# Performance work log

Hardware: AMD Instinct MI355X
Metric: run time of the kernel (lower is better)

## Reference

```python
import jax, jax.numpy as jnp
import numpy as np

T = 2048; H = 1024; NH = 16; NKV = 4; HD = 64
E = 32; TOPK = 4; NG = 4; TG = 2; IM = 384; ISH = 384
ROT = HD // 2          # partial_rotary_factor = 0.5
EPS = 1e-5; RSF = 1.0; THETA = 10000.0


def setup_inputs() -> dict:
    ks = jax.random.split(jax.random.key(0), 12)
    g = lambda k, sh, sc=0.02: jax.random.normal(k, sh, jnp.float32) * sc
    return {
        "hidden_states": g(ks[0], (T, H), 1.0),
        "residual": g(ks[1], (T, H), 1.0),
        "in_ln_w": jnp.ones((H,), jnp.float32),
        "post_ln_w": jnp.ones((H,), jnp.float32),
        "q_norm_w": jnp.ones((HD,), jnp.float32),
        "k_norm_w": jnp.ones((HD,), jnp.float32),
        "Wqkv": g(ks[2], (H, (NH + 2 * NKV) * HD)),
        "Wo": g(ks[3], (NH * HD, H)),
        "Wg": g(ks[4], (H, E)),
        "gate_bias": g(ks[5], (E,), 0.1),
        "Wgu": g(ks[6], (E, H, 2 * IM)),
        "Wd": g(ks[7], (E, IM, H)),
        "Wgu_sh": g(ks[8], (H, 2 * ISH)),
        "Wd_sh": g(ks[9], (ISH, H)),
        "positions": jnp.arange(T, dtype=jnp.int32),
    }


def _rms(x, w):
    return x * jax.lax.rsqrt(jnp.mean(x * x, -1, keepdims=True) + EPS) * w


def _rope(x, pos):
    # neox-style rotary on the first ROT dims of each head; x: [T, nheads, HD]
    half = ROT // 2
    inv = THETA ** (-(jnp.arange(half, dtype=jnp.float32) * 2.0 / ROT))
    ang = pos.astype(jnp.float32)[:, None] * inv          # [T, half]
    c = jnp.cos(ang)[:, None, :]
    s = jnp.sin(ang)[:, None, :]
    x1, x2, rest = x[..., :half], x[..., half:ROT], x[..., ROT:]
    return jnp.concatenate([x1 * c - x2 * s, x1 * s + x2 * c, rest], -1)


def _layer(pos, hidden, residual, in_ln_w, post_ln_w, q_norm_w, k_norm_w,
           Wqkv, Wo, Wg, gate_bias, Wgu, Wd, Wgu_sh, Wd_sh):
    # fused add-RMSNorm (vllm RMSNorm(x, residual))
    residual = hidden + residual
    hidden = _rms(residual, in_ln_w)

    # self-attention (GQA, per-head qk-norm, partial rotary, causal)
    qkv = hidden @ Wqkv
    q = qkv[:, :NH * HD].reshape(T, NH, HD)
    k = qkv[:, NH * HD:(NH + NKV) * HD].reshape(T, NKV, HD)
    v = qkv[:, (NH + NKV) * HD:].reshape(T, NKV, HD)
    q = _rms(q, q_norm_w)
    k = _rms(k, k_norm_w)
    q = _rope(q, pos)
    k = _rope(k, pos)
    rep = NH // NKV
    k = jnp.repeat(k, rep, axis=1)
    v = jnp.repeat(v, rep, axis=1)
    scores = jnp.einsum('thd,shd->hts', q, k) * (HD ** -0.5)
    causal = pos[:, None] >= pos[None, :]
    scores = jnp.where(causal[None], scores, -jnp.inf)
    attn = jax.nn.softmax(scores, axis=-1)
    o = jnp.einsum('hts,shd->thd', attn, v).reshape(T, NH * HD)
    hidden = o @ Wo

    # post-attention fused add-RMSNorm
    residual = hidden + residual
    hidden = _rms(residual, post_ln_w)

    # --- Glm4MoE: grouped sigmoid top-k router with e_score_correction_bias ---
    logits = hidden.astype(jnp.float32) @ Wg            # gate runs in fp32
    scr = jax.nn.sigmoid(logits)                        # [T, E]
    sfc = scr + gate_bias                               # scores_for_choice
    # group score = sum of top-2 biased scores within each group
    gs = jnp.sum(jax.lax.top_k(sfc.reshape(T, NG, E // NG), 2)[0], -1)  # [T, NG]
    _, gidx = jax.lax.top_k(gs, TG)
    gmask = jnp.zeros((T, NG), jnp.float32).at[jnp.arange(T)[:, None], gidx].set(1.0)
    emask = jnp.repeat(gmask, E // NG, axis=1)          # [T, E]
    _, ids = jax.lax.top_k(jnp.where(emask > 0, sfc, -jnp.inf), TOPK)
    w = jnp.take_along_axis(scr, ids, axis=1)           # weights from unbiased scores
    w = w / jnp.sum(w, -1, keepdims=True)               # renormalize (norm_topk_prob)
    wdense = jnp.zeros((T, E), jnp.float32).at[jnp.arange(T)[:, None], ids].set(w)

    # routed experts: dense-over-experts reference for the grouped GEMM dispatch
    gu = jnp.einsum('th,ehi->tei', hidden, Wgu)         # [T, E, 2*IM]
    act = jax.nn.silu(gu[..., :IM]) * gu[..., IM:]      # SiluAndMul
    routed = jnp.einsum('te,tei,eih->th', wdense, act, Wd)

    # shared expert MLP
    gus = hidden @ Wgu_sh
    shared = (jax.nn.silu(gus[:, :ISH]) * gus[:, ISH:]) @ Wd_sh

    hidden = routed * RSF + shared
    return hidden, residual


def reference(hidden_states, residual, in_ln_w, post_ln_w, q_norm_w, k_norm_w,
              Wqkv, Wo, Wg, gate_bias, Wgu, Wd, Wgu_sh, Wd_sh, positions):
    return _layer(positions, hidden_states, residual, in_ln_w, post_ln_w,
                  q_norm_w, k_norm_w, Wqkv, Wo, Wg, gate_bias, Wgu, Wd,
                  Wgu_sh, Wd_sh)
```

## Files before the change

kernel.cpp:

```cpp
#include <hip/hip_runtime.h>
#include <math.h>

#define TT 2048
#define HH 1024
#define NHEADS 16
#define NKVH 4
#define HDIM 64
#define NEXP 32
#define TOPK_ 4
#define NGRP 4
#define IMID 384
#define ISHARED 384
#define QKV_W (24*64)
#define EPS_ 1e-5f
#define MAXSB 288
#define NSPLITS 80

typedef __attribute__((ext_vector_type(8))) short short8;
typedef __attribute__((ext_vector_type(4))) float f32x4;

__device__ __forceinline__ ushort f2bf(float x) {
  union { float f; unsigned u; } v; v.f = x;
  unsigned r = v.u + 0x7fffu + ((v.u >> 16) & 1u);
  return (ushort)(r >> 16);
}
__device__ __forceinline__ float bf2f(ushort u) {
  union { unsigned i; float f; } v; v.i = (unsigned)u << 16; return v.f;
}

__device__ __forceinline__ void gload16(const void* g, void* l) {
  __builtin_amdgcn_global_load_lds(
      (const __attribute__((address_space(1))) unsigned int*)g,
      (__attribute__((address_space(3))) unsigned int*)l, 16, 0, 0);
}

__device__ __forceinline__ short8 read_a_frag32(const ushort* As, int lg, int row) {
  return *(const short8*)(As + ((lg * 32 + (row ^ lg)) * 8));
}
__device__ __forceinline__ short8 read_a_frag64(const ushort* As, int lg, int row) {
  return *(const short8*)(As + ((lg * 64 + (row ^ lg)) * 8));
}
__device__ __forceinline__ short8 read_b_frag(const ushort* Bs, int lg, int col) {
  int boff = (col * 16) ^ (((col >> 3) & 7) << 4);
  return *(const short8*)((const char*)Bs + lg * 1024 + boff);
}

__device__ __forceinline__ void stage_B_tile(const float* __restrict__ B, int ldb,
                                             int k0, int col0, ushort* Bs, int tid) {
  int a = tid >> 4;
  int cG = tid & 15;
  int k = 2 * a;
  const float* p0 = B + (size_t)(k0 + k) * ldb + col0 + cG * 4;
  const float* p1 = p0 + ldb;
  float4 r0 = *(const float4*)p0;
  float4 r1 = *(const float4*)p1;
  int gg = (k & 15) >> 2;
  int slot = (k & 3) + ((k >> 4) << 2);
  float v0[4] = {r0.x, r0.y, r0.z, r0.w};
  float v1[4] = {r1.x, r1.y, r1.z, r1.w};
  char* plane = (char*)Bs + gg * 1024;
  #pragma unroll
  for (int j = 0; j < 4; ++j) {
    int c = cG * 4 + j;
    unsigned pk = (unsigned)f2bf(v0[j]) | ((unsigned)f2bf(v1[j]) << 16);
    int boff = ((c * 16) ^ (((c >> 3) & 7) << 4)) + slot * 2;
    *(unsigned*)(plane + boff) = pk;
  }
}

__global__ __launch_bounds__(256) void pack_B_kernel(
    const float* __restrict__ src, ushort* __restrict__ dst, int N) {
  __shared__ ushort tileB[2048];
  int tid = threadIdx.x;
  stage_B_tile(src, N, blockIdx.y * 32, blockIdx.x * 64, tileB, tid);
  __syncthreads();
  size_t toff = ((size_t)blockIdx.y * gridDim.x + blockIdx.x) * 2048;
  *(short8*)(dst + toff + tid * 8) = *(const short8*)(tileB + tid * 8);
}

__global__ __launch_bounds__(256) void gemm64_bb(
    const ushort* __restrict__ Ab, const ushort* __restrict__ Bpk,
    float* __restrict__ C, int M, int N, int K) {
  __shared__ ushort As[4][2048];
  __shared__ ushort Bs[4][2048];
  int tid = threadIdx.x;
  int row0 = blockIdx.y * 64, col0 = blockIdx.x * 64;
  int ntn = N >> 6;
  int wid = tid >> 6, lane = tid & 63;
  int lg = lane >> 4, lr = lane & 15;
  int wrow = (wid >> 1) * 32, wcol = (wid & 1) * 32;
  const ushort* asrc = Ab + (size_t)(row0 + (lane ^ wid)) * K + wid * 8;
  const ushort* bsrc = Bpk + (size_t)blockIdx.x * 2048 + wid * 512 + lane * 8;
  const int NT = K >> 5;
  f32x4 acc[2][2] = {};

  auto issue = [&](int tt) {
    int b = tt & 3;
    gload16(asrc + tt * 32, &As[b][wid * 512]);
    gload16(bsrc + (size_t)tt * ntn * 2048, &Bs[b][wid * 512]);
  };
  issue(0); issue(1); issue(2);
  for (int t = 0; t < NT; ++t) {
    int ahead = NT - 1 - t;
    if (ahead >= 2)      asm volatile("s_waitcnt vmcnt(4)" ::: "memory");
    else if (ahead == 1) asm volatile("s_waitcnt vmcnt(2)" ::: "memory");
    else                 asm volatile("s_waitcnt vmcnt(0)" ::: "memory");
    __builtin_amdgcn_s_barrier();
    if (t + 3 < NT) issue(t + 3);
    int cb = t & 3;
    short8 af0 = read_a_frag64(&As[cb][0], lg, wrow + lr);
    short8 af1 = read_a_frag64(&As[cb][0], lg, wrow + 16 + lr);
    #pragma unroll
    for (int nn = 0; nn < 2; ++nn) {
      short8 bf_ = read_b_frag(&Bs[cb][0], lg, wcol + nn * 16 + lr);
      acc[0][nn] = __builtin_amdgcn_mfma_f32_16x16x32_bf16(af0, bf_, acc[0][nn], 0, 0, 0);
      acc[1][nn] = __builtin_amdgcn_mfma_f32_16x16x32_bf16(af1, bf_, acc[1][nn], 0, 0, 0);
    }
  }
  #pragma unroll
  for (int mm = 0; mm < 2; ++mm)
    #pragma unroll
    for (int nn = 0; nn < 2; ++nn) {
      int row = row0 + wrow + mm * 16 + lg * 4;
      int col = col0 + wcol + nn * 16 + lr;
      #pragma unroll
      for (int i = 0; i < 4; ++i)
        C[(size_t)(row + i) * N + col] = acc[mm][nn][i];
    }
}

__global__ __launch_bounds__(256) void moe_up_pk(
    const ushort* __restrict__ hln2b, const ushort* __restrict__ Wpk,
    const int* __restrict__ perm, const int* __restrict__ offs,
    const int* __restrict__ counts, const int* __restrict__ sb_e,
    const int* __restrict__ sb_base, const int* __restrict__ nsb,
    ushort* __restrict__ actb) {
  int b = blockIdx.x;
  int sb = ((b & 7) * 36) + (b >> 3);
  if (sb >= *nsb) return;
  int e = sb_e[sb];
  int base = sb_base[sb];
  int start = offs[e];
  int nt = min(32, counts[e] - base);
  __shared__ int tokmap[32];
  int tid = threadIdx.x;
  if (tid < 32) tokmap[tid] = perm[start + base + ((tid < nt) ? tid : 0)] >> 2;
  __shared__ ushort As[3][1024];
  __shared__ ushort Bg[3][2048];
  __shared__ ushort Bu[3][2048];
  __syncthreads();
  int bz = blockIdx.y, col0 = bz * 64;
  int wid = tid >> 6, lane = tid & 63;
  int lg = lane >> 4, lr = lane & 15;
  int wrow = (wid >> 1) * 16, wcol = (wid & 1) * 32;
  const ushort* bgt = Wpk + ((size_t)(e * 32) * 12 + bz) * 2048 + wid * 512 + lane * 8;
  const ushort* but = bgt + (size_t)6 * 2048;
  int ga = wid * 2 + (lane >> 5);
  const ushort* asrcA = hln2b + (size_t)tokmap[(lane & 31) ^ ga] * HH + ga * 8;
  const int NT = HH >> 5;
  f32x4 accg[2] = {}, accu[2] = {};

  auto issue = [&](int tt) {
    int bb = tt % 3;
    if (wid < 2) gload16(asrcA + tt * 32, &As[bb][wid * 1024 / 2]);
    gload16(bgt + (size_t)tt * 12 * 2048, &Bg[bb][wid * 512]);
    gload16(but + (size_t)tt * 12 * 2048, &Bu[bb][wid * 512]);
  };
  issue(0); issue(1);
  for (int t = 0; t < NT; ++t) {
    if (t < NT - 1) {
      if (wid < 2) asm volatile("s_waitcnt vmcnt(3)" ::: "memory");
      else         asm volatile("s_waitcnt vmcnt(2)" ::: "memory");
    } else {
      asm volatile("s_waitcnt vmcnt(0)" ::: "memory");
    }
    __builtin_amdgcn_s_barrier();
    if (t + 2 < NT) issue(t + 2);
    int cb = t % 3;
    short8 af = read_a_frag32(&As[cb][0], lg, wrow + lr);
    #pragma unroll
    for (int nn = 0; nn < 2; ++nn) {
      short8 bgf = read_b_frag(&Bg[cb][0], lg, wcol + nn * 16 + lr);
      short8 buf_ = read_b_frag(&Bu[cb][0], lg, wcol + nn * 16 + lr);
      accg[nn] = __builtin_amdgcn_mfma_f32_16x16x32_bf16(af, bgf, accg[nn], 0, 0, 0);
      accu[nn] = __builtin_amdgcn_mfma_f32_16x16x32_bf16(af, buf_, accu[nn], 0, 0, 0);
    }
  }
  #pragma unroll
  for (int nn = 0; nn < 2; ++nn) {
    int pcol = col0 + ((wid & 1) << 5) + ((lr >> 2) << 3) + (nn << 2) + (lr & 3);
    #pragma unroll
    for (int i = 0; i < 4; ++i) {
      int rr = wrow + lg * 4 + i;
      if (rr < nt) {
        float gv = accg[nn][i], uv = accu[nn][i];
        float av = gv / (1.f + expf(-gv)) * uv;
        actb[(size_t)(start + base + rr) * IMID + pcol] = f2bf(av);
      }
    }
  }
}

__global__ __launch_bounds__(256) void moe_down_pk(
    const ushort* __restrict__ actb, const ushort* __restrict__ Wpk,
    const int* __restrict__ offs, const int* __restrict__ counts,
    const int* __restrict__ sb_e, const int* __restrict__ sb_base,
    const int* __restrict__ nsb, ushort* __restrict__ partialb) {
  int b = blockIdx.x;
  int sb = ((b & 7) * 36) + (b >> 3);
  if (sb >= *nsb) return;
  int e = sb_e[sb];
  int base = sb_base[sb];
  int start = offs[e];
  int nt = min(32, counts[e] - base);
  __shared__ ushort As[3][1024];
  __shared__ ushort Bs[3][2048];
  int tid = threadIdx.x;
  int bz = blockIdx.y, col0 = bz * 64;
  int wid = tid >> 6, lane = tid & 63;
  int lg = lane >> 4, lr = lane & 15;
  int wrow = (wid >> 1) * 16, wcol = (wid & 1) * 32;
  const ushort* bt0 = Wpk + ((size_t)(e * 12) * 16 + bz) * 2048 + wid * 512 + lane * 8;
  int ga = wid * 2 + (lane >> 5);
  const ushort* asrcA = actb + (size_t)(start + base + ((lane & 31) ^ ga)) * IMID + ga * 8;
  const int NT = IMID >> 5;
  f32x4 acc[2] = {};

  auto issue = [&](int tt) {
    int bb = tt % 3;
    if (wid < 2) gload16(asrcA + tt * 32, &As[bb][wid * 512]);
    gload16(bt0 + (size_t)tt * 16 * 2048, &Bs[bb][wid * 512]);
  };
  issue(0); issue(1);
  for (int t = 0; t < NT; ++t) {
    if (t < NT - 1) {
      if (wid < 2) asm volatile("s_waitcnt vmcnt(2)" ::: "memory");
      else         asm volatile("s_waitcnt vmcnt(1)" ::: "memory");
    } else {
      asm volatile("s_waitcnt vmcnt(0)" ::: "memory");
    }
    __builtin_amdgcn_s_barrier();
    if (t + 2 < NT) issue(t + 2);
    int cb = t % 3;
    short8 af = read_a_frag32(&As[cb][0], lg, wrow + lr);
    #pragma unroll
    for (int nn = 0; nn < 2; ++nn) {
      short8 bf_ = read_b_frag(&Bs[cb][0], lg, wcol + nn * 16 + lr);
      acc[nn] = __builtin_amdgcn_mfma_f32_16x16x32_bf16(af, bf_, acc[nn], 0, 0, 0);
    }
  }
  #pragma unroll
  for (int nn = 0; nn < 2; ++nn)
    #pragma unroll
    for (int i = 0; i < 4; ++i) {
      int rr = wrow + lg * 4 + i;
      if (rr < nt)
        partialb[(size_t)(start + base + rr) * HH + col0 + wcol + nn * 16 + lr] = f2bf(acc[nn][i]);
    }
}

__global__ __launch_bounds__(256) void add_rms_kernel(
    const float* __restrict__ a, const float* __restrict__ b,
    const float* __restrict__ w, float* __restrict__ sum_out,
    float* __restrict__ ln_out, ushort* __restrict__ lnb) {
  int t = blockIdx.x, tid = threadIdx.x;
  float4 x = reinterpret_cast<const float4*>(a + (size_t)t*HH)[tid];
  float4 y = reinterpret_cast<const float4*>(b + (size_t)t*HH)[tid];
  x.x += y.x; x.y += y.y; x.z += y.z; x.w += y.w;
  float ss = x.x*x.x + x.y*x.y + x.z*x.z + x.w*x.w;
  #pragma unroll
  for (int off = 1; off < 64; off <<= 1) ss += __shfl_xor(ss, off);
  __shared__ float wsum[4];
  int wid = tid >> 6, lane = tid & 63;
  if (lane == 0) wsum[wid] = ss;
  __syncthreads();
  float tot = wsum[0] + wsum[1] + wsum[2] + wsum[3];
  float r = rsqrtf(tot * (1.0f/HH) + EPS_);
  reinterpret_cast<float4*>(sum_out + (size_t)t*HH)[tid] = x;
  float4 wl = reinterpret_cast<const float4*>(w)[tid];
  float4 o = make_float4(x.x*r*wl.x, x.y*r*wl.y, x.z*r*wl.z, x.w*r*wl.w);
  reinterpret_cast<float4*>(ln_out + (size_t)t*HH)[tid] = o;
  ushort4 ub;
  ub.x = f2bf(o.x); ub.y = f2bf(o.y); ub.z = f2bf(o.z); ub.w = f2bf(o.w);
  int dst = ((tid >> 3) << 5) + ((tid & 3) << 3) + (((tid >> 2) & 1) << 2);
  *(ushort4*)(lnb + (size_t)t * HH + dst) = ub;
}

__global__ __launch_bounds__(256) void qk_norm_rope_kernel(
    float* __restrict__ qkv, const float* __restrict__ qw,
    const float* __restrict__ kw, const int* __restrict__ pos) {
  int t = blockIdx.x;
  int hh = blockIdx.y * 4 + (threadIdx.x >> 6);
  int lane = threadIdx.x & 63;
  float* p = qkv + (size_t)t * QKV_W + hh * HDIM;
  float x = p[lane];
  float ss = x * x;
  #pragma unroll
  for (int off = 1; off < 64; off <<= 1) ss += __shfl_xor(ss, off);
  float r = rsqrtf(ss * (1.0f/HDIM) + EPS_);
  float wv = (hh < NHEADS ? qw : kw)[lane];
  float xn = x * r * wv;
  float partner = __shfl_xor(xn, 16);
  float out = xn;
  if (lane < 32) {
    int i = lane & 15;
    float inv = powf(10000.0f, -(float)i / 16.0f);
    float ang = (float)pos[t] * inv;
    float cv = cosf(ang), sv = sinf(ang);
    out = (lane < 16) ? (xn * cv - partner * sv) : (partner * sv + xn * cv);
  }
  p[lane] = out;
}

__global__ __launch_bounds__(256) void pack_KV_kernel(
    const float* __restrict__ qkv, ushort* __restrict__ Kpk,
    ushort* __restrict__ Vpk) {
  __shared__ ushort kimg[2048];
  __shared__ ushort vimg[2048];
  int tid = threadIdx.x;
  int kt = blockIdx.x, kvh = blockIdx.y;
  {
    int c = tid >> 7, t2 = tid & 127;
    int g = t2 & 3, r = t2 >> 2;
    const float* kp = qkv + (size_t)(kt*32 + r) * QKV_W + NHEADS*HDIM + kvh*HDIM + 32*c + 4*g;
    float4 h0 = *(const float4*)kp;
    float4 h1 = *(const float4*)(kp + 16);
    short8 v;
    v[0]=(short)f2bf(h0.x); v[1]=(short)f2bf(h0.y); v[2]=(short)f2bf(h0.z); v[3]=(short)f2bf(h0.w);
    v[4]=(short)f2bf(h1.x); v[5]=(short)f2bf(h1.y); v[6]=(short)f2bf(h1.z); v[7]=(short)f2bf(h1.w);
    *(short8*)(kimg + c*1024 + (g*32 + (r^g))*8) = v;
  }
  stage_B_tile(qkv + (size_t)(NHEADS+NKVH)*HDIM + (size_t)kvh*HDIM, QKV_W, kt*32, 0, vimg, tid);
  __syncthreads();
  size_t toff = ((size_t)(kvh * (TT/32) + kt)) * 2048;
  *(short8*)(Kpk + toff + tid * 8) = *(const short8*)(kimg + tid * 8);
  *(short8*)(Vpk + toff + tid * 8) = *(const short8*)(vimg + tid * 8);
}

__global__ __launch_bounds__(256) void attn_v3_kernel(
    const float* __restrict__ qkv, const ushort* __restrict__ Kpk,
    const ushort* __restrict__ Vpk, ushort* __restrict__ ob,
    float* __restrict__ po, float* __restrict__ pl) {
  __shared__ ushort Ks[3][2048];
  __shared__ ushort Vs[3][2048];
  int tid = threadIdx.x;
  int wid = tid >> 6, lane = tid & 63;
  int lg = lane >> 4, lr = lane & 15;
  int h = blockIdx.y;
  int f = blockIdx.x;
  int g = 0;
  while (f >= 4 * (g + 1) * (g + 2)) ++g;
  int r_ = f - 4 * g * (g + 1);
  int ns = g + 1;
  int qb = 8 * g + r_ / ns;
  int s = r_ % ns;
  int tiles_total = 2 * qb + 2;
  int per = (tiles_total + ns - 1) / ns;
  int lo = s * per;
  int nloc = min(per, tiles_total - lo);
  int kvh = h >> 2;
  int q0 = qb * 64 + wid * 16;
  int qg = q0 + lr;
  const float SCL = 0.125f * 1.44269504f;
  const float FM = 16.0f;

  const float* qrow = qkv + (size_t)qg * QKV_W + h * HDIM;
  short8 qfr[2];
  #pragma unroll
  for (int c = 0; c < 2; ++c) {
    float4 a = *(const float4*)(qrow + 32*c + 4*lg);
    float4 b = *(const float4*)(qrow + 32*c + 4*lg + 16);
    short8 v;
    v[0]=(short)f2bf(a.x*SCL); v[1]=(short)f2bf(a.y*SCL); v[2]=(short)f2bf(a.z*SCL); v[3]=(short)f2bf(a.w*SCL);
    v[4]=(short)f2bf(b.x*SCL); v[5]=(short)f2bf(b.y*SCL); v[6]=(short)f2bf(b.z*SCL); v[7]=(short)f2bf(b.w*SCL);
    qfr[c] = v;
  }

  const ushort* ksrc = Kpk + (size_t)(kvh * (TT/32) + lo) * 2048 + wid * 512 + lane * 8;
  const ushort* vsrc = Vpk + (size_t)(kvh * (TT/32) + lo) * 2048 + wid * 512 + lane * 8;

  f32x4 o_acc[4] = {};
  float l_st = 0.f;

  auto issue = [&](int tt) {
    int b = tt % 3;
    gload16(ksrc + (size_t)tt * 2048, &Ks[b][wid * 512]);
    gload16(vsrc + (size_t)tt * 2048, &Vs[b][wid * 512]);
  };
  issue(0);
  if (nloc > 1) issue(1);
  for (int tt = 0; tt < nloc; ++tt) {
    if (tt < nloc - 1) asm volatile("s_waitcnt vmcnt(2)" ::: "memory");
    else               asm volatile("s_waitcnt vmcnt(0)" ::: "memory");
    __builtin_amdgcn_s_barrier();
    if (tt + 2 < nloc) issue(tt + 2);
    int t = lo + tt;
    if (t * 32 > q0 + 15) continue;
    int cb = tt % 3;
    f32x4 st[2];
    #pragma unroll
    for (int n = 0; n < 2; ++n) {
      short8 kf0 = *(const short8*)(&Ks[cb][(lg*32 + ((16*n + lr) ^ lg)) * 8]);
      short8 kf1 = *(const short8*)(&Ks[cb][1024 + (lg*32 + ((16*n + lr) ^ lg)) * 8]);
      f32x4 z = {};
      z = __builtin_amdgcn_mfma_f32_16x16x32_bf16(kf0, qfr[0], z, 0, 0, 0);
      st[n] = __builtin_amdgcn_mfma_f32_16x16x32_bf16(kf1, qfr[1], z, 0, 0, 0);
    }
    float p[2][4];
    float psum = 0.f;
    if (t * 32 + 31 <= q0) {
      #pragma unroll
      for (int n = 0; n < 2; ++n)
        #pragma unroll
        for (int i = 0; i < 4; ++i) {
          float pv = exp2f(st[n][i] - FM);
          p[n][i] = pv; psum += pv;
        }
    } else {
      #pragma unroll
      for (int n = 0; n < 2; ++n)
        #pragma unroll
        for (int i = 0; i < 4; ++i) {
          int kvg = t*32 + 16*n + 4*lg + i;
          float pv = (kvg <= qg) ? exp2f(st[n][i] - FM) : 0.f;
          p[n][i] = pv; psum += pv;
        }
    }
    psum += __shfl_xor(psum, 16);
    psum += __shfl_xor(psum, 32);
    l_st += psum;
    union { unsigned u[4]; short8 s8; } pu;
    asm volatile("v_cvt_pk_bf16_f32 %0, %1, %2" : "=v"(pu.u[0]) : "v"(p[0][0]), "v"(p[0][1]));
    asm volatile("v_cvt_pk_bf16_f32 %0, %1, %2" : "=v"(pu.u[1]) : "v"(p[0][2]), "v"(p[0][3]));
    asm volatile("v_cvt_pk_bf16_f32 %0, %1, %2" : "=v"(pu.u[2]) : "v"(p[1][0]), "v"(p[1][1]));
    asm volatile("v_cvt_pk_bf16_f32 %0, %1, %2" : "=v"(pu.u[3]) : "v"(p[1][2]), "v"(p[1][3]));
    short8 pa = pu.s8;
    #pragma unroll
    for (int nd = 0; nd < 4; ++nd) {
      short8 vf = read_b_frag(&Vs[cb][0], lg, 16*nd + lr);
      o_acc[nd] = __builtin_amdgcn_mfma_f32_16x16x32_bf16(pa, vf, o_acc[nd], 0, 0, 0);
    }
  }

  if (ns == 1) {
    #pragma unroll
    for (int i = 0; i < 4; ++i) {
      float lrow = __shfl(l_st, 4*lg + i);
      float inv = 1.0f / lrow;
      int row = q0 + 4*lg + i;
      ushort* op = ob + (size_t)row * (NHEADS*HDIM) + h * HDIM;
      #pragma unroll
      for (int nd = 0; nd < 4; ++nd) {
        int pcol = ((nd >> 1) << 5) + ((lr >> 2) << 3) + ((nd & 1) << 2) + (lr & 3);
        op[pcol] = f2bf(o_acc[nd][i] * inv);
      }
    }
  } else {
    float* pob = po + ((size_t)f * NHEADS + h) * 4096;
    #pragma unroll
    for (int nd = 0; nd < 4; ++nd)
      #pragma unroll
      for (int i = 0; i < 4; ++i)
        pob[(wid * 16 + lg * 4 + i) * 64 + 16 * nd + lr] = o_acc[nd][i];
    if (lg == 0)
      pl[((size_t)f * NHEADS + h) * 64 + wid * 16 + lr] = l_st;
  }
}

__global__ __launch_bounds__(256) void attn_combine_kernel(
    const float* __restrict__ po, const float* __restrict__ pl,
    ushort* __restrict__ ob) {
  int h = blockIdx.x;
  int qb = 8 + blockIdx.y;
  int g = qb >> 3;
  int ns = g + 1;
  int f0 = 4 * g * (g + 1) + (qb - 8 * g) * ns;
  int tid = threadIdx.x;
  int r = tid >> 2, c = tid & 3;
  float acc[16] = {};
  float lsum = 0.f;
  for (int s = 0; s < ns; ++s) {
    size_t base = ((size_t)(f0 + s) * NHEADS + h) * 4096 + r * 64 + c * 16;
    #pragma unroll
    for (int j = 0; j < 4; ++j) {
      float4 v = *(const float4*)(po + base + j * 4);
      acc[j*4+0] += v.x; acc[j*4+1] += v.y; acc[j*4+2] += v.z; acc[j*4+3] += v.w;
    }
    lsum += pl[((size_t)(f0 + s) * NHEADS + h) * 64 + r];
  }
  float inv = 1.0f / lsum;
  int row = qb * 64 + r;
  ushort* op = ob + (size_t)row * (NHEADS*HDIM) + h * HDIM + (c >> 1) * 32 + (c & 1) * 4;
  #pragma unroll
  for (int a = 0; a < 4; ++a) {
    ushort4 u;
    u.x = f2bf(acc[a*4+0] * inv); u.y = f2bf(acc[a*4+1] * inv);
    u.z = f2bf(acc[a*4+2] * inv); u.w = f2bf(acc[a*4+3] * inv);
    *(ushort4*)(op + a * 8) = u;
  }
}

__global__ __launch_bounds__(256) void router_kernel(
    const float* __restrict__ hln, const float* __restrict__ Wg,
    const float* __restrict__ bias, int* __restrict__ sel_e,
    float* __restrict__ sel_w) {
  __shared__ float hid[4][HH];
  int tid = threadIdx.x, wid = tid >> 6, lane = tid & 63;
  int t = blockIdx.x * 4 + wid;
  const float4* src = (const float4*)(hln + (size_t)t * HH);
  float4* dst = (float4*)hid[wid];
  #pragma unroll
  for (int j = 0; j < 4; ++j) dst[j * 64 + lane] = src[j * 64 + lane];
  int e = lane & 31, half = lane >> 5;
  const float* wp = Wg + (size_t)(half * 512) * NEXP + e;
  const float* hp = hid[wid] + half * 512;
  float p = 0.f;
  #pragma unroll 8
  for (int h = 0; h < 512; ++h) p += hp[h] * wp[(size_t)h * NEXP];
  p += __shfl_xor(p, 32);
  float sc = 1.0f / (1.0f + expf(-p));
  float sfc = sc + bias[e];
  float m1 = sfc, m2 = -1e30f;
  #pragma unroll
  for (int off = 1; off <= 4; off <<= 1) {
    float om1 = __shfl_xor(m1, off), om2 = __shfl_xor(m2, off);
    float hi_ = fmaxf(m1, om1);
    float lo_ = fmaxf(fminf(m1, om1), fmaxf(m2, om2));
    m1 = hi_; m2 = lo_;
  }
  float gs = m1 + m2;
  float gv[4] = {__shfl(gs, 0), __shfl(gs, 8), __shfl(gs, 16), __shfl(gs, 24)};
  int g1 = 0; float b1 = gv[0];
  #pragma unroll
  for (int g = 1; g < 4; ++g) if (gv[g] > b1) { b1 = gv[g]; g1 = g; }
  int g2 = -1; float b2 = -1e30f;
  #pragma unroll
  for (int g = 0; g < 4; ++g) if (g != g1 && gv[g] > b2) { b2 = gv[g]; g2 = g; }
  bool keep = ((e >> 3) == g1) || ((e >> 3) == g2);
  float cand = keep ? sfc : -1e30f;
  int ids[4]; float wv[4]; float wsum = 0.f;
  #pragma unroll
  for (int s = 0; s < 4; ++s) {
    float v = cand; int ix = e;
    #pragma unroll
    for (int off = 1; off < 64; off <<= 1) {
      float ov = __shfl_xor(v, off); int oix = __shfl_xor(ix, off);
      if (ov > v || (ov == v && oix < ix)) { v = ov; ix = oix; }
    }
    ids[s] = ix;
    if (e == ix) cand = -1e30f;
    float w = __shfl(sc, ix);
    wv[s] = w; wsum += w;
  }
  if (lane == 0) {
    #pragma unroll
    for (int s = 0; s < 4; ++s) {
      sel_e[t * 4 + s] = ids[s];
      sel_w[t * 4 + s] = wv[s] / wsum;
    }
  }
}

__global__ __launch_bounds__(256) void count_kernel(
    const int* __restrict__ sel_e, int* __restrict__ counts) {
  int e = blockIdx.x, tid = threadIdx.x;
  int c = 0;
  for (int i = tid; i < TT * TOPK_; i += 256) c += (sel_e[i] == e);
  #pragma unroll
  for (int off = 1; off < 64; off <<= 1) c += __shfl_xor(c, off);
  __shared__ int wsum[4];
  if ((tid & 63) == 0) wsum[tid >> 6] = c;
  __syncthreads();
  if (tid == 0) counts[e] = wsum[0] + wsum[1] + wsum[2] + wsum[3];
}

__global__ void scan_kernel(const int* __restrict__ counts,
                            int* __restrict__ offs, int* __restrict__ cursor,
                            int* __restrict__ sb_e, int* __restrict__ sb_base,
                            int* __restrict__ nsb) {
  if (threadIdx.x == 0) {
    int acc = 0, n = 0;
    for (int e = 0; e < NEXP; ++e) {
      offs[e] = acc; cursor[e] = acc;
      int c = counts[e];
      for (int b = 0; b < c; b += 32) { sb_e[n] = e; sb_base[n] = b; ++n; }
      acc += c;
    }
    *nsb = n;
  }
}

__global__ void scatter_kernel(const int* __restrict__ sel_e,
                               int* __restrict__ cursor, int* __restrict__ perm,
                               int* __restrict__ ipos) {
  int i = blockIdx.x * 256 + threadIdx.x;
  if (i < TT * TOPK_) {
    int e = sel_e[i];
    int pos = atomicAdd(&cursor[e], 1);
    perm[pos] = i;
    ipos[i] = pos;
  }
}

__global__ __launch_bounds__(256) void silu_shared_kernel(
    const float* __restrict__ gus, ushort* __restrict__ shsb) {
  int i = blockIdx.x * 256 + threadIdx.x;
  if (i < TT * (ISHARED/4)) {
    int t = i / (ISHARED/4), k = i % (ISHARED/4);
    const float* gp = gus + (size_t)t * (2*ISHARED) + k * 4;
    float4 g4 = *(const float4*)gp;
    float4 u4 = *(const float4*)(gp + ISHARED);
    ushort4 r;
    r.x = f2bf(g4.x / (1.f + expf(-g4.x)) * u4.x);
    r.y = f2bf(g4.y / (1.f + expf(-g4.y)) * u4.y);
    r.z = f2bf(g4.z / (1.f + expf(-g4.z)) * u4.z);
    r.w = f2bf(g4.w / (1.f + expf(-g4.w)) * u4.w);
    int pdst = ((k >> 3) << 5) + ((k & 3) << 3) + (((k >> 2) & 1) << 2);
    *(ushort4*)(shsb + (size_t)t * ISHARED + pdst) = r;
  }
}

__global__ __launch_bounds__(256) void final_combine_kernel(
    const ushort* __restrict__ partialb, const float* __restrict__ sel_w,
    const int* __restrict__ ipos, const float* __restrict__ shared_out,
    float* __restrict__ out_hidden) {
  int t = blockIdx.x, tid = threadIdx.x;
  float w0 = sel_w[t*4], w1 = sel_w[t*4+1], w2 = sel_w[t*4+2], w3 = sel_w[t*4+3];
  int p0 = ipos[t*4], p1 = ipos[t*4+1], p2 = ipos[t*4+2], p3 = ipos[t*4+3];
  ushort4 a0 = *(const ushort4*)(partialb + (size_t)p0*HH + tid*4);
  ushort4 a1 = *(const ushort4*)(partialb + (size_t)p1*HH + tid*4);
  ushort4 a2 = *(const ushort4*)(partialb + (size_t)p2*HH + tid*4);
  ushort4 a3 = *(const ushort4*)(partialb + (size_t)p3*HH + tid*4);
  float4 sh = reinterpret_cast<const float4*>(shared_out + (size_t)t*HH)[tid];
  float4 r;
  r.x = (w0*bf2f(a0.x) + w1*bf2f(a1.x) + w2*bf2f(a2.x) + w3*bf2f(a3.x)) + sh.x;
  r.y = (w0*bf2f(a0.y) + w1*bf2f(a1.y) + w2*bf2f(a2.y) + w3*bf2f(a3.y)) + sh.y;
  r.z = (w0*bf2f(a0.z) + w1*bf2f(a1.z) + w2*bf2f(a2.z) + w3*bf2f(a3.z)) + sh.z;
  r.w = (w0*bf2f(a0.w) + w1*bf2f(a1.w) + w2*bf2f(a2.w) + w3*bf2f(a3.w)) + sh.w;
  reinterpret_cast<float4*>(out_hidden + (size_t)t*HH)[tid] = r;
}

extern "C" void kernel_launch(void* const* d_in, const int* in_sizes, int n_in,
                              void* d_out, int out_size, void* d_ws, size_t ws_size,
                              hipStream_t stream) {
  const float* hidden   = (const float*)d_in[0];
  const float* residual = (const float*)d_in[1];
  const float* in_ln_w  = (const float*)d_in[2];
  const float* post_ln_w= (const float*)d_in[3];
  const float* q_norm_w = (const float*)d_in[4];
  const float* k_norm_w = (const float*)d_in[5];
  const float* Wqkv     = (const float*)d_in[6];
  const float* Wo       = (const float*)d_in[7];
  const float* Wg       = (const float*)d_in[8];
  const float* gate_bias= (const float*)d_in[9];
  const float* Wgu      = (const float*)d_in[10];
  const float* Wd       = (const float*)d_in[11];
  const float* Wgu_sh   = (const float*)d_in[12];
  const float* Wd_sh    = (const float*)d_in[13];
  const int*   positions= (const int*)d_in[14];
  float* out = (float*)d_out;

  float* f = (float*)d_ws;
  size_t off = 0;
  float* R_A   = f + off; off += (size_t)TT*HH;
  float* HLN   = f + off; off += (size_t)TT*HH;
  float* QKV   = f + off; off += (size_t)TT*QKV_W;
  float* OATT  = f + off; off += (size_t)TT*HH;
  float* HLN2  = f + off; off += (size_t)TT*HH;
  float* SELW  = f + off; off += (size_t)TT*TOPK_;
  float* PO    = f + off; off += (size_t)NSPLITS*NHEADS*4096;
  float* PL    = f + off; off += (size_t)NSPLITS*NHEADS*64;
  ushort* HLNB  = (ushort*)(f + off); off += (size_t)TT*HH/2;
  ushort* HLN2B = (ushort*)(f + off); off += (size_t)TT*HH/2;
  ushort* OATTB = (ushort*)(f + off); off += (size_t)TT*HH/2;
  ushort* SHSB  = (ushort*)(f + off); off += (size_t)TT*ISHARED/2;
  ushort* KPK   = (ushort*)(f + off); off += (size_t)NKVH*(TT/32)*2048/2;
  ushort* VPK   = (ushort*)(f + off); off += (size_t)NKVH*(TT/32)*2048/2;
  ushort* ACTB  = (ushort*)(f + off); off += (size_t)(TT*TOPK_ + 128)*IMID/2;
  ushort* PARTB = (ushort*)(f + off); off += (size_t)TT*TOPK_*HH/2;
  ushort* PK_QKV = (ushort*)(f + off); off += (size_t)HH*QKV_W/2;
  ushort* PK_WO  = (ushort*)(f + off); off += (size_t)HH*HH/2;
  ushort* PK_WGU = (ushort*)(f + off); off += (size_t)NEXP*HH*(2*IMID)/2;
  ushort* PK_WD  = (ushort*)(f + off); off += (size_t)NEXP*IMID*HH/2;
  ushort* PK_GUSH= (ushort*)(f + off); off += (size_t)HH*(2*ISHARED)/2;
  ushort* PK_DSH = (ushort*)(f + off); off += (size_t)ISHARED*HH/2;
  int* ibase   = (int*)(f + off);
  int* SELE    = ibase;
  int* PERM    = ibase + TT*TOPK_;
  int* IPOS    = ibase + 2*TT*TOPK_;
  int* COUNTS  = ibase + 3*TT*TOPK_;
  int* OFFS    = COUNTS + NEXP;
  int* CURSOR  = OFFS + NEXP;
  int* SB_E    = CURSOR + NEXP;
  int* SB_BASE = SB_E + MAXSB;
  int* NSB     = SB_BASE + MAXSB;

  pack_B_kernel<<<dim3(QKV_W/64, HH/32), 256, 0, stream>>>(Wqkv, PK_QKV, QKV_W);
  pack_B_kernel<<<dim3(HH/64, HH/32), 256, 0, stream>>>(Wo, PK_WO, HH);
  pack_B_kernel<<<dim3((2*IMID)/64, NEXP*HH/32), 256, 0, stream>>>(Wgu, PK_WGU, 2*IMID);
  pack_B_kernel<<<dim3(HH/64, NEXP*IMID/32), 256, 0, stream>>>(Wd, PK_WD, HH);
  pack_B_kernel<<<dim3((2*ISHARED)/64, HH/32), 256, 0, stream>>>(Wgu_sh, PK_GUSH, 2*ISHARED);
  pack_B_kernel<<<dim3(HH/64, ISHARED/32), 256, 0, stream>>>(Wd_sh, PK_DSH, HH);

  add_rms_kernel<<<TT, 256, 0, stream>>>(hidden, residual, in_ln_w, R_A, HLN, HLNB);
  gemm64_bb<<<dim3(QKV_W/64, TT/64), 256, 0, stream>>>(HLNB, PK_QKV, QKV, TT, QKV_W, HH);
  qk_norm_rope_kernel<<<dim3(TT, 5), 256, 0, stream>>>(QKV, q_norm_w, k_norm_w, positions);
  pack_KV_kernel<<<dim3(TT/32, NKVH), 256, 0, stream>>>(QKV, KPK, VPK);
  attn_v3_kernel<<<dim3(NSPLITS, NHEADS), 256, 0, stream>>>(QKV, KPK, VPK, OATTB, PO, PL);
  attn_combine_kernel<<<dim3(NHEADS, 24), 256, 0, stream>>>(PO, PL, OATTB);
  gemm64_bb<<<dim3(HH/64, TT/64), 256, 0, stream>>>(OATTB, PK_WO, HLN, TT, HH, HH);
  add_rms_kernel<<<TT, 256, 0, stream>>>(HLN, R_A, post_ln_w, out + (size_t)TT*HH, HLN2, HLN2B);
  router_kernel<<<TT/4, 256, 0, stream>>>(HLN2, Wg, gate_bias, SELE, SELW);
  count_kernel<<<NEXP, 256, 0, stream>>>(SELE, COUNTS);
  scan_kernel<<<1, 64, 0, stream>>>(COUNTS, OFFS, CURSOR, SB_E, SB_BASE, NSB);
  scatter_kernel<<<(TT*TOPK_ + 255)/256, 256, 0, stream>>>(SELE, CURSOR, PERM, IPOS);
  moe_up_pk<<<dim3(MAXSB, IMID/64), 256, 0, stream>>>(HLN2B, PK_WGU, PERM, OFFS, COUNTS, SB_E, SB_BASE, NSB, ACTB);
  moe_down_pk<<<dim3(MAXSB, HH/64), 256, 0, stream>>>(ACTB, PK_WD, OFFS, COUNTS, SB_E, SB_BASE, NSB, PARTB);
  gemm64_bb<<<dim3((2*ISHARED)/64, TT/64), 256, 0, stream>>>(HLN2B, PK_GUSH, QKV, TT, 2*ISHARED, HH);
  silu_shared_kernel<<<(TT*(ISHARED/4) + 255)/256, 256, 0, stream>>>(QKV, SHSB);
  gemm64_bb<<<dim3(HH/64, TT/64), 256, 0, stream>>>(SHSB, PK_DSH, OATT, TT, HH, ISHARED);
  final_combine_kernel<<<TT, 256, 0, stream>>>(PARTB, SELW, IPOS, OATT, out);
}
```

Baseline: 350.0 us.

## Drop LDS staging in MoE expert GEMMs; load fragments directly to registers

The MoE up and down kernels no longer stage A and B tiles through triple-buffered shared memory with barriers. Each wave now reads its MFMA fragments straight from global memory into registers, with one-step register prefetch. Each wave computes a 32x32 output tile, so the grid's y-dimension is halved. This removes LDS traffic and barrier synchronisation, but each wave fetches its own copy of the A data rather than sharing it across the block, and relies on cache hits and latency hiding from register prefetch.

```diff
diff --git a/kernel.cpp b/kernel.cpp
--- a/kernel.cpp
+++ b/kernel.cpp
@@ -34,9 +34,6 @@
       (__attribute__((address_space(3))) unsigned int*)l, 16, 0, 0);
 }
 
-__device__ __forceinline__ short8 read_a_frag32(const ushort* As, int lg, int row) {
-  return *(const short8*)(As + ((lg * 32 + (row ^ lg)) * 8));
-}
 __device__ __forceinline__ short8 read_a_frag64(const ushort* As, int lg, int row) {
   return *(const short8*)(As + ((lg * 64 + (row ^ lg)) * 8));
 }
@@ -142,63 +139,66 @@
   int base = sb_base[sb];
   int start = offs[e];
   int nt = min(32, counts[e] - base);
-  __shared__ int tokmap[32];
   int tid = threadIdx.x;
-  if (tid < 32) tokmap[tid] = perm[start + base + ((tid < nt) ? tid : 0)] >> 2;
-  __shared__ ushort As[3][1024];
-  __shared__ ushort Bg[3][2048];
-  __shared__ ushort Bu[3][2048];
-  __syncthreads();
-  int bz = blockIdx.y, col0 = bz * 64;
   int wid = tid >> 6, lane = tid & 63;
   int lg = lane >> 4, lr = lane & 15;
-  int wrow = (wid >> 1) * 16, wcol = (wid & 1) * 32;
-  const ushort* bgt = Wpk + ((size_t)(e * 32) * 12 + bz) * 2048 + wid * 512 + lane * 8;
-  const ushort* but = bgt + (size_t)6 * 2048;
-  int ga = wid * 2 + (lane >> 5);
-  const ushort* asrcA = hln2b + (size_t)tokmap[(lane & 31) ^ ga] * HH + ga * 8;
-  const int NT = HH >> 5;
-  f32x4 accg[2] = {}, accu[2] = {};
-
-  auto issue = [&](int tt) {
-    int bb = tt % 3;
-    if (wid < 2) gload16(asrcA + tt * 32, &As[bb][wid * 1024 / 2]);
-    gload16(bgt + (size_t)tt * 12 * 2048, &Bg[bb][wid * 512]);
-    gload16(but + (size_t)tt * 12 * 2048, &Bu[bb][wid * 512]);
-  };
-  issue(0); issue(1);
-  for (int t = 0; t < NT; ++t) {
-    if (t < NT - 1) {
-      if (wid < 2) asm volatile("s_waitcnt vmcnt(3)" ::: "memory");
-      else         asm volatile("s_waitcnt vmcnt(2)" ::: "memory");
-    } else {
-      asm volatile("s_waitcnt vmcnt(0)" ::: "memory");
-    }
-    __builtin_amdgcn_s_barrier();
-    if (t + 2 < NT) issue(t + 2);
-    int cb = t % 3;
-    short8 af = read_a_frag32(&As[cb][0], lg, wrow + lr);
+  int bz = blockIdx.y * 2 + (wid >> 1);
+  int wcol = (wid & 1) * 32;
+  int tok0 = perm[start + base + min(lr, nt - 1)] >> 2;
+  int tok1 = perm[start + base + min(16 + lr, nt - 1)] >> 2;
+  const ushort* a0p = hln2b + (size_t)tok0 * HH + lg * 8;
+  const ushort* a1p = hln2b + (size_t)tok1 * HH + lg * 8;
+  int c0 = wcol + lr, c1 = wcol + 16 + lr;
+  int sw0 = (c0 * 16) ^ (((c0 >> 3) & 7) << 4);
+  int sw1 = (c1 * 16) ^ (((c1 >> 3) & 7) << 4);
+  const char* gbase = (const char*)Wpk + ((size_t)(e * 32) * 12 + bz) * 4096 + lg * 1024;
+  const char* ubase = gbase + (size_t)6 * 4096;
+  const size_t bstep = (size_t)12 * 4096;
+  f32x4 accg[2][2] = {}, accu[2][2] = {};
+  short8 a0c = *(const short8*)(a0p);
+  short8 a1c = *(const short8*)(a1p);
+  short8 g0c = *(const short8*)(gbase + sw0);
+  short8 g1c = *(const short8*)(gbase + sw1);
+  short8 u0c = *(const short8*)(ubase + sw0);
+  short8 u1c = *(const short8*)(ubase + sw1);
+  #pragma unroll 4
+  for (int t = 0; t < 32; ++t) {
+    short8 a0n = a0c, a1n = a1c, g0n = g0c, g1n = g1c, u0n = u0c, u1n = u1c;
+    if (t < 31) {
+      const char* gb = gbase + (size_t)(t + 1) * bstep;
+      const char* ub = ubase + (size_t)(t + 1) * bstep;
+      a0n = *(const short8*)(a0p + (t + 1) * 32);
+      a1n = *(const short8*)(a1p + (t + 1) * 32);
+      g0n = *(const short8*)(gb + sw0);
+      g1n = *(const short8*)(gb + sw1);
+      u0n = *(const short8*)(ub + sw0);
+      u1n = *(const short8*)(ub + sw1);
+    }
+    accg[0][0] = __builtin_amdgcn_mfma_f32_16x16x32_bf16(a0c, g0c, accg[0][0], 0, 0, 0);
+    accg[0][1] = __builtin_amdgcn_mfma_f32_16x16x32_bf16(a0c, g1c, accg[0][1], 0, 0, 0);
+    accg[1][0] = __builtin_amdgcn_mfma_f32_16x16x32_bf16(a1c, g0c, accg[1][0], 0, 0, 0);
+    accg[1][1] = __builtin_amdgcn_mfma_f32_16x16x32_bf16(a1c, g1c, accg[1][1], 0, 0, 0);
+    accu[0][0] = __builtin_amdgcn_mfma_f32_16x16x32_bf16(a0c, u0c, accu[0][0], 0, 0, 0);
+    accu[0][1] = __builtin_amdgcn_mfma_f32_16x16x32_bf16(a0c, u1c, accu[0][1], 0, 0, 0);
+    accu[1][0] = __builtin_amdgcn_mfma_f32_16x16x32_bf16(a1c, u0c, accu[1][0], 0, 0, 0);
+    accu[1][1] = __builtin_amdgcn_mfma_f32_16x16x32_bf16(a1c, u1c, accu[1][1], 0, 0, 0);
+    a0c = a0n; a1c = a1n; g0c = g0n; g1c = g1n; u0c = u0n; u1c = u1n;
+  }
+  #pragma unroll
+  for (int mm = 0; mm < 2; ++mm)
     #pragma unroll
     for (int nn = 0; nn < 2; ++nn) {
-      short8 bgf = read_b_frag(&Bg[cb][0], lg, wcol + nn * 16 + lr);
-      short8 buf_ = read_b_frag(&Bu[cb][0], lg, wcol + nn * 16 + lr);
-      accg[nn] = __builtin_amdgcn_mfma_f32_16x16x32_bf16(af, bgf, accg[nn], 0, 0, 0);
-      accu[nn] = __builtin_amdgcn_mfma_f32_16x16x32_bf16(af, buf_, accu[nn], 0, 0, 0);
-    }
-  }
-  #pragma unroll
-  for (int nn = 0; nn < 2; ++nn) {
-    int pcol = col0 + ((wid & 1) << 5) + ((lr >> 2) << 3) + (nn << 2) + (lr & 3);
-    #pragma unroll
-    for (int i = 0; i < 4; ++i) {
-      int rr = wrow + lg * 4 + i;
-      if (rr < nt) {
-        float gv = accg[nn][i], uv = accu[nn][i];
-        float av = gv / (1.f + expf(-gv)) * uv;
-        actb[(size_t)(start + base + rr) * IMID + pcol] = f2bf(av);
+      int pcol = bz * 64 + wcol + ((lr >> 2) << 3) + (nn << 2) + (lr & 3);
+      #pragma unroll
+      for (int i = 0; i < 4; ++i) {
+        int rr = mm * 16 + lg * 4 + i;
+        if (rr < nt) {
+          float gv = accg[mm][nn][i], uv = accu[mm][nn][i];
+          float av = gv / (1.f + expf(-gv)) * uv;
+          actb[(size_t)(start + base + rr) * IMID + pcol] = f2bf(av);
+        }
       }
     }
-  }
 }
 
 __global__ __launch_bounds__(256) void moe_down_pk(
@@ -213,50 +213,49 @@
   int base = sb_base[sb];
   int start = offs[e];
   int nt = min(32, counts[e] - base);
-  __shared__ ushort As[3][1024];
-  __shared__ ushort Bs[3][2048];
   int tid = threadIdx.x;
-  int bz = blockIdx.y, col0 = bz * 64;
   int wid = tid >> 6, lane = tid & 63;
   int lg = lane >> 4, lr = lane & 15;
-  int wrow = (wid >> 1) * 16, wcol = (wid & 1) * 32;
-  const ushort* bt0 = Wpk + ((size_t)(e * 12) * 16 + bz) * 2048 + wid * 512 + lane * 8;
-  int ga = wid * 2 + (lane >> 5);
-  const ushort* asrcA = actb + (size_t)(start + base + ((lane & 31) ^ ga)) * IMID + ga * 8;
-  const int NT = IMID >> 5;
-  f32x4 acc[2] = {};
-
-  auto issue = [&](int tt) {
-    int bb = tt % 3;
-    if (wid < 2) gload16(asrcA + tt * 32, &As[bb][wid * 512]);
-    gload16(bt0 + (size_t)tt * 16 * 2048, &Bs[bb][wid * 512]);
-  };
-  issue(0); issue(1);
-  for (int t = 0; t < NT; ++t) {
-    if (t < NT - 1) {
-      if (wid < 2) asm volatile("s_waitcnt vmcnt(2)" ::: "memory");
-      else         asm volatile("s_waitcnt vmcnt(1)" ::: "memory");
-    } else {
-      asm volatile("s_waitcnt vmcnt(0)" ::: "memory");
-    }
-    __builtin_amdgcn_s_barrier();
-    if (t + 2 < NT) issue(t + 2);
-    int cb = t % 3;
-    short8 af = read_a_frag32(&As[cb][0], lg, wrow + lr);
-    #pragma unroll
-    for (int nn = 0; nn < 2; ++nn) {
-      short8 bf_ = read_b_frag(&Bs[cb][0], lg, wcol + nn * 16 + lr);
-      acc[nn] = __builtin_amdgcn_mfma_f32_16x16x32_bf16(af, bf_, acc[nn], 0, 0, 0);
-    }
-  }
-  #pragma unroll
-  for (int nn = 0; nn < 2; ++nn)
-    #pragma unroll
-    for (int i = 0; i < 4; ++i) {
-      int rr = wrow + lg * 4 + i;
-      if (rr < nt)
-        partialb[(size_t)(start + base + rr) * HH + col0 + wcol + nn * 16 + lr] = f2bf(acc[nn][i]);
-    }
+  int nct = blockIdx.y * 2 + (wid >> 1);
+  int wcol = (wid & 1) * 32;
+  const ushort* a0p = actb + (size_t)(start + base + min(lr, nt - 1)) * IMID + lg * 8;
+  const ushort* a1p = actb + (size_t)(start + base + min(16 + lr, nt - 1)) * IMID + lg * 8;
+  int c0 = wcol + lr, c1 = wcol + 16 + lr;
+  int sw0 = (c0 * 16) ^ (((c0 >> 3) & 7) << 4);
+  int sw1 = (c1 * 16) ^ (((c1 >> 3) & 7) << 4);
+  const char* bbase = (const char*)Wpk + ((size_t)(e * 12) * 16 + nct) * 4096 + lg * 1024;
+  const size_t bstep = (size_t)16 * 4096;
+  f32x4 acc[2][2] = {};
+  short8 a0c = *(const short8*)(a0p);
+  short8 a1c = *(const short8*)(a1p);
+  short8 b0c = *(const short8*)(bbase + sw0);
+  short8 b1c = *(const short8*)(bbase + sw1);
+  #pragma unroll 4
+  for (int t = 0; t < 12; ++t) {
+    short8 a0n = a0c, a1n = a1c, b0n = b0c, b1n = b1c;
+    if (t < 11) {
+      const char* bb = bbase + (size_t)(t + 1) * bstep;
+      a0n = *(const short8*)(a0p + (t + 1) * 32);
+      a1n = *(const short8*)(a1p + (t + 1) * 32);
+      b0n = *(const short8*)(bb + sw0);
+      b1n = *(const short8*)(bb + sw1);
+    }
+    acc[0][0] = __builtin_amdgcn_mfma_f32_16x16x32_bf16(a0c, b0c, acc[0][0], 0, 0, 0);
+    acc[0][1] = __builtin_amdgcn_mfma_f32_16x16x32_bf16(a0c, b1c, acc[0][1], 0, 0, 0);
+    acc[1][0] = __builtin_amdgcn_mfma_f32_16x16x32_bf16(a1c, b0c, acc[1][0], 0, 0, 0);
+    acc[1][1] = __builtin_amdgcn_mfma_f32_16x16x32_bf16(a1c, b1c, acc[1][1], 0, 0, 0);
+    a0c = a0n; a1c = a1n; b0c = b0n; b1c = b1n;
+  }
+  #pragma unroll
+  for (int mm = 0; mm < 2; ++mm)
+    #pragma unroll
+    for (int nn = 0; nn < 2; ++nn)
+      #pragma unroll
+      for (int i = 0; i < 4; ++i) {
+        int rr = mm * 16 + lg * 4 + i;
+        if (rr < nt)
+          partialb[(size_t)(start + base + rr) * HH + nct * 64 + wcol + nn * 16 + lr] = f2bf(acc[mm][nn][i]);
+      }
 }
 
 __global__ __launch_bounds__(256) void add_rms_kernel(
@@ -714,8 +713,8 @@
   count_kernel<<<NEXP, 256, 0, stream>>>(SELE, COUNTS);
   scan_kernel<<<1, 64, 0, stream>>>(COUNTS, OFFS, CURSOR, SB_E, SB_BASE, NSB);
   scatter_kernel<<<(TT*TOPK_ + 255)/256, 256, 0, stream>>>(SELE, CURSOR, PERM, IPOS);
-  moe_up_pk<<<dim3(MAXSB, IMID/64), 256, 0, stream>>>(HLN2B, PK_WGU, PERM, OFFS, COUNTS, SB_E, SB_BASE, NSB, ACTB);
-  moe_down_pk<<<dim3(MAXSB, HH/64), 256, 0, stream>>>(ACTB, PK_WD, OFFS, COUNTS, SB_E, SB_BASE, NSB, PARTB);
+  moe_up_pk<<<dim3(MAXSB, 3), 256, 0, stream>>>(HLN2B, PK_WGU, PERM, OFFS, COUNTS, SB_E, SB_BASE, NSB, ACTB);
+  moe_down_pk<<<dim3(MAXSB, 8), 256, 0, stream>>>(ACTB, PK_WD, OFFS, COUNTS, SB_E, SB_BASE, NSB, PARTB);
   gemm64_bb<<<dim3((2*ISHARED)/64, TT/64), 256, 0, stream>>>(HLN2B, PK_GUSH, QKV, TT, 2*ISHARED, HH);
   silu_shared_kernel<<<(TT*(ISHARED/4) + 255)/256, 256, 0, stream>>>(QKV, SHSB);
   gemm64_bb<<<dim3(HH/64, TT/64), 256, 0, stream>>>(SHSB, PK_DSH, OATT, TT, HH, ISHARED);
```

After: 363.5 us. 3.9% more time.
